# Kernel tuning notes

Measured on AMD Instinct MI355X. Metric: run time of the kernel, lower is better.

The kernel has to match this reference:

```python
import jax, jax.numpy as jnp
import numpy as np

B, S, HID = 2, 1024, 2048
N_HEADS, N_KV, HEAD_DIM = 32, 4, 128
BLOCK, MAX_BLOCKS = 32, 128
EPS = 1e-6
ROPE_THETA = 1e6


def _rmsnorm(x, w):
    # per-head RMSNorm over head_dim (Qwen3MoeRMSNorm)
    var = jnp.mean(x * x, axis=-1, keepdims=True)
    return x * jax.lax.rsqrt(var + EPS) * w


def _rotate_half(x):
    h = x.shape[-1] // 2
    return jnp.concatenate([-x[..., h:], x[..., :h]], axis=-1)


def setup_inputs() -> dict:
    key = jax.random.key(0)
    ks = jax.random.split(key, 8)
    hidden_states = jax.random.normal(ks[0], (B, S, HID), dtype=jnp.float32)
    wq = jax.random.normal(ks[1], (N_HEADS * HEAD_DIM, HID), dtype=jnp.float32) * 0.02
    wk = jax.random.normal(ks[2], (N_KV * HEAD_DIM, HID), dtype=jnp.float32) * 0.02
    wv = jax.random.normal(ks[3], (N_KV * HEAD_DIM, HID), dtype=jnp.float32) * 0.02
    wo = jax.random.normal(ks[4], (HID, N_HEADS * HEAD_DIM), dtype=jnp.float32) * 0.02
    q_norm_w = 1.0 + 0.01 * jax.random.normal(ks[5], (HEAD_DIM,), dtype=jnp.float32)
    k_norm_w = 1.0 + 0.01 * jax.random.normal(ks[6], (HEAD_DIM,), dtype=jnp.float32)
    # RoPE tables (rotate-half / llama convention)
    inv_freq = 1.0 / (ROPE_THETA ** (jnp.arange(0, HEAD_DIM, 2, dtype=jnp.float32) / HEAD_DIM))
    t = jnp.arange(S, dtype=jnp.float32)
    freqs = jnp.outer(t, inv_freq)  # [S, HEAD_DIM/2]
    emb = jnp.concatenate([freqs, freqs], axis=-1)  # [S, HEAD_DIM]
    cos, sin = jnp.cos(emb), jnp.sin(emb)
    # page table: B sequences x (S/BLOCK) blocks, distinct block ids
    page_table = jnp.arange(B * (S // BLOCK), dtype=jnp.int32).reshape(B, S // BLOCK)
    return {"hidden_states": hidden_states, "wq": wq, "wk": wk, "wv": wv, "wo": wo,
            "q_norm_w": q_norm_w, "k_norm_w": k_norm_w, "cos": cos, "sin": sin,
            "page_table": page_table}


def reference(hidden_states, wq, wk, wv, wo, q_norm_w, k_norm_w, cos, sin, page_table):
    b, s, _ = hidden_states.shape
    # fused QKV projection (math-equivalent to the concatenated qkv_proj_weight)
    q = (hidden_states @ wq.T).reshape(b, s, N_HEADS, HEAD_DIM)
    k = (hidden_states @ wk.T).reshape(b, s, N_KV, HEAD_DIM)
    v = (hidden_states @ wv.T).reshape(b, s, N_KV, HEAD_DIM)
    # per-head RMSNorm then RoPE
    q = _rmsnorm(q, q_norm_w)
    k = _rmsnorm(k, k_norm_w)
    c = cos[None, :, None, :]
    sn = sin[None, :, None, :]
    q = q * c + _rotate_half(q) * sn
    k = k * c + _rotate_half(k) * sn
    # paged KV-cache fill: [B, nblk, BLOCK, kvh, hd] -> cache[block_id, kvh, BLOCK, hd]
    nblk = s // BLOCK
    k_blk = k.reshape(b, nblk, BLOCK, N_KV, HEAD_DIM).transpose(0, 1, 3, 2, 4).reshape(-1, N_KV, BLOCK, HEAD_DIM)
    v_blk = v.reshape(b, nblk, BLOCK, N_KV, HEAD_DIM).transpose(0, 1, 3, 2, 4).reshape(-1, N_KV, BLOCK, HEAD_DIM)
    flat_pt = page_table.reshape(-1)
    cache_k = jnp.zeros((MAX_BLOCKS, N_KV, BLOCK, HEAD_DIM), dtype=k.dtype).at[flat_pt].set(k_blk)
    cache_v = jnp.zeros((MAX_BLOCKS, N_KV, BLOCK, HEAD_DIM), dtype=v.dtype).at[flat_pt].set(v_blk)
    # GQA: repeat kv heads (num_key_value_groups = 8)
    groups = N_HEADS // N_KV
    k_rep = jnp.repeat(k, groups, axis=2)  # [b, s, N_HEADS, hd]
    v_rep = jnp.repeat(v, groups, axis=2)
    # causal SDPA, scaling = head_dim ** -0.5
    scale = HEAD_DIM ** -0.5
    scores = jnp.einsum('bqhd,bkhd->bhqk', q, k_rep) * scale
    causal = jnp.tril(jnp.ones((s, s), dtype=bool))
    scores = jnp.where(causal[None, None], scores, jnp.finfo(scores.dtype).min)
    probs = jax.nn.softmax(scores, axis=-1)
    attn = jnp.einsum('bhqk,bkhd->bqhd', probs, v_rep).reshape(b, s, N_HEADS * HEAD_DIM)
    out = attn @ wo.T  # [b, s, HID]
    return out, cache_k, cache_v
```

## Files before the change

### kernel.cpp

```cpp
#include <hip/hip_runtime.h>
#include <hip/hip_bf16.h>


typedef __attribute__((ext_vector_type(8))) __bf16 bf16x8;
typedef __attribute__((ext_vector_type(4))) __bf16 bf16x4;
typedef __attribute__((ext_vector_type(4))) float f32x4;

__device__ __forceinline__ void gload16(const void* g, void* l) {
    __builtin_amdgcn_global_load_lds((const __attribute__((address_space(1))) void*)g,
                                     (__attribute__((address_space(3))) void*)l, 16, 0, 0);
}

__global__ __launch_bounds__(256) void cvt5(const float* __restrict__ s0, const float* __restrict__ s1,
                                            const float* __restrict__ s2, const float* __restrict__ s3,
                                            const float* __restrict__ s4,
                                            __bf16* __restrict__ d0, __bf16* __restrict__ d1,
                                            __bf16* __restrict__ d2, __bf16* __restrict__ d3,
                                            __bf16* __restrict__ d4) {
    const int b = blockIdx.x;
    const float* src; __bf16* dst; int off;
    if (b < 4096)       { src = s0; dst = d0; off = b; }
    else if (b < 12288) { src = s1; dst = d1; off = b - 4096; }
    else if (b < 13312) { src = s2; dst = d2; off = b - 12288; }
    else if (b < 14336) { src = s3; dst = d3; off = b - 13312; }
    else                { src = s4; dst = d4; off = b - 14336; }
    const int i = off * 256 + threadIdx.x;
    float4 v = reinterpret_cast<const float4*>(src)[i];
    bf16x4 o = {(__bf16)v.x, (__bf16)v.y, (__bf16)v.z, (__bf16)v.w};
    reinterpret_cast<bf16x4*>(dst)[i] = o;
}

__global__ __launch_bounds__(256) void reduce_add(float* __restrict__ o,
                                                  const float* __restrict__ p, int n4) {
    int i = blockIdx.x * 256 + threadIdx.x;
    int stride = gridDim.x * 256;
    for (; i < n4; i += stride) {
        float4 a = reinterpret_cast<float4*>(o)[i];
        float4 b = reinterpret_cast<const float4*>(p)[i];
        a.x += b.x; a.y += b.y; a.z += b.z; a.w += b.w;
        reinterpret_cast<float4*>(o)[i] = a;
    }
}

template <int NF, int OUT_BF16>
__global__ __launch_bounds__(512, 2) void gemm4p(const __bf16* __restrict__ A,
                                                 const __bf16* __restrict__ B,
                                                 void* __restrict__ C0,
                                                 void* __restrict__ C1,
                                                 const int M, const int N, const int K,
                                                 const int nTiles, const int nbn,
                                                 const int klen) {
    __shared__ __bf16 Asm[2 * 128 * 64];
    __shared__ __bf16 Bsm[2 * NF * 64 * 64];
    const int tid = threadIdx.x, lane = tid & 63, wave = tid >> 6;
    const int wm = wave >> 2, wn = wave & 3;
    const int lrow = lane & 15, lkg = lane >> 4;
    const int rsw = lrow & 7;
    const int bid = blockIdx.x;
    const int kz = bid / nTiles, tile = bid % nTiles;
    const int tswz = (tile & 7) * (nTiles >> 3) + (tile >> 3);
    const int bm = tswz / nbn, bn = tswz % nbn;
    const int brow = bm * 128, bcol = bn * (NF * 64);
    const int kbeg = kz * klen;
    const int row0 = tid >> 3;
    const int scol_sw = ((tid & 7) ^ (row0 & 7)) * 8;
    const __bf16* gA = A + (size_t)(brow + row0) * K + kbeg + scol_sw;
    const __bf16* gB = B + (size_t)(bcol + row0) * K + kbeg + scol_sw;
    const int slot0 = (lkg ^ rsw) * 8;
    const int slot1 = ((4 + lkg) ^ rsw) * 8;
    const int nt = klen / 64;
    constexpr int UPT = NF + 2;

    f32x4 acc[4][NF] = {};

    int su_t = 0, su_w = 0;
    auto stage1 = [&]() {
        if (su_t < nt) {
            const size_t ko = (size_t)su_t * 64;
            if (su_w < 2)
                gload16(gA + (size_t)(su_w * 64) * K + ko,
                        Asm + (su_t & 1) * 8192 + su_w * 4096 + tid * 8);
            else
                gload16(gB + (size_t)((su_w - 2) * 64) * K + ko,
                        Bsm + (su_t & 1) * (NF * 4096) + (su_w - 2) * 4096 + tid * 8);
        }
        if (++su_w == UPT) { su_w = 0; ++su_t; }
    };

    for (int u = 0; u < 2 * UPT; ++u) stage1();
    if constexpr (NF == 5) asm volatile("s_waitcnt vmcnt(7)" ::: "memory");
    else                   asm volatile("s_waitcnt vmcnt(6)" ::: "memory");
    __builtin_amdgcn_s_barrier();

    for (int t = 0; t < nt; ++t) {
        const __bf16* As = Asm + (t & 1) * 8192;
        const __bf16* Bs = Bsm + (t & 1) * (NF * 4096);
        bf16x8 ar[4], br[NF];
#pragma unroll
        for (int mi = 0; mi < 4; ++mi)
            ar[mi] = *reinterpret_cast<const bf16x8*>(&As[(wm * 64 + mi * 16 + lrow) * 64 + slot0]);
#pragma unroll
        for (int nf = 0; nf < NF; ++nf)
            br[nf] = *reinterpret_cast<const bf16x8*>(&Bs[(wn * (NF * 16) + nf * 16 + lrow) * 64 + slot0]);
        asm volatile("s_waitcnt lgkmcnt(0)" ::: "memory");
        __builtin_amdgcn_sched_barrier(0);
        __builtin_amdgcn_s_setprio(1);
#pragma unroll
        for (int mi = 0; mi < 4; ++mi)
#pragma unroll
            for (int nf = 0; nf < NF; ++nf)
                acc[mi][nf] = __builtin_amdgcn_mfma_f32_16x16x32_bf16(ar[mi], br[nf], acc[mi][nf], 0, 0, 0);
        __builtin_amdgcn_s_setprio(0);
        __builtin_amdgcn_s_barrier();
#pragma unroll
        for (int mi = 0; mi < 4; ++mi)
            ar[mi] = *reinterpret_cast<const bf16x8*>(&As[(wm * 64 + mi * 16 + lrow) * 64 + slot1]);
#pragma unroll
        for (int nf = 0; nf < NF; ++nf)
            br[nf] = *reinterpret_cast<const bf16x8*>(&Bs[(wn * (NF * 16) + nf * 16 + lrow) * 64 + slot1]);
        asm volatile("s_waitcnt lgkmcnt(0)" ::: "memory");
#pragma unroll
        for (int u = 0; u < UPT; ++u) stage1();
        __builtin_amdgcn_sched_barrier(0);
        __builtin_amdgcn_s_setprio(1);
#pragma unroll
        for (int mi = 0; mi < 4; ++mi)
#pragma unroll
            for (int nf = 0; nf < NF; ++nf)
                acc[mi][nf] = __builtin_amdgcn_mfma_f32_16x16x32_bf16(ar[mi], br[nf], acc[mi][nf], 0, 0, 0);
        __builtin_amdgcn_s_setprio(0);
        if (t + 2 < nt) {
            if constexpr (NF == 5) asm volatile("s_waitcnt vmcnt(7)" ::: "memory");
            else                   asm volatile("s_waitcnt vmcnt(6)" ::: "memory");
        } else {
            asm volatile("s_waitcnt vmcnt(0)" ::: "memory");
        }
        __builtin_amdgcn_s_barrier();
    }

    void* C = (kz == 0) ? C0 : C1;
#pragma unroll
    for (int mi = 0; mi < 4; ++mi)
#pragma unroll
        for (int nf = 0; nf < NF; ++nf)
#pragma unroll
            for (int j = 0; j < 4; ++j) {
                const size_t r = brow + wm * 64 + mi * 16 + lkg * 4 + j;
                const size_t c = bcol + wn * (NF * 16) + nf * 16 + lrow;
                if (OUT_BF16)
                    ((__bf16*)C)[r * N + c] = (__bf16)acc[mi][nf][j];
                else
                    ((float*)C)[r * N + c] = acc[mi][nf][j];
            }
}

__global__ __launch_bounds__(256) void norm_rope_cache(
    __bf16* __restrict__ qkv, const float* __restrict__ cosT, const float* __restrict__ sinT,
    const float* __restrict__ qw, const float* __restrict__ kw,
    const int* __restrict__ ptab, float* __restrict__ cacheK, float* __restrict__ cacheV) {
    const int t = blockIdx.x;
    const int b = t >> 10, s = t & 1023;
    const int wave = threadIdx.x >> 6, lane = threadIdx.x & 63;
    __bf16* row = qkv + (size_t)t * 5120;
    const float c = cosT[s * 128 + lane];
    const float sn = sinT[s * 128 + lane];
    const int page = ptab[b * 32 + (s >> 5)];
    const int so = s & 31;
    const float wq0 = qw[lane], wq1 = qw[lane + 64];
#pragma unroll
    for (int i = 0; i < 8; ++i) {
        const int h = wave * 8 + i;
        float x0 = (float)row[h * 128 + lane];
        float x1 = (float)row[h * 128 + 64 + lane];
        float ss = x0 * x0 + x1 * x1;
        for (int off = 32; off; off >>= 1) ss += __shfl_xor(ss, off);
        const float rs = rsqrtf(ss * (1.0f / 128.0f) + 1e-6f);
        const float y0 = x0 * rs * wq0, y1 = x1 * rs * wq1;
        row[h * 128 + lane]      = (__bf16)(y0 * c - y1 * sn);
        row[h * 128 + 64 + lane] = (__bf16)(y1 * c + y0 * sn);
    }
    {
        const int h = wave;
        float x0 = (float)row[4096 + h * 128 + lane];
        float x1 = (float)row[4096 + h * 128 + 64 + lane];
        float ss = x0 * x0 + x1 * x1;
        for (int off = 32; off; off >>= 1) ss += __shfl_xor(ss, off);
        const float rs = rsqrtf(ss * (1.0f / 128.0f) + 1e-6f);
        const float y0 = x0 * rs * kw[lane], y1 = x1 * rs * kw[lane + 64];
        const float o0 = y0 * c - y1 * sn, o1 = y1 * c + y0 * sn;
        row[4096 + h * 128 + lane]      = (__bf16)o0;
        row[4096 + h * 128 + 64 + lane] = (__bf16)o1;
        float* ck = cacheK + (((size_t)page * 4 + h) * 32 + so) * 128;
        ck[lane] = o0; ck[lane + 64] = o1;
        const float v0 = (float)row[4608 + h * 128 + lane];
        const float v1 = (float)row[4608 + h * 128 + 64 + lane];
        float* cv = cacheV + (((size_t)page * 4 + h) * 32 + so) * 128;
        cv[lane] = v0; cv[lane + 64] = v1;
    }
}

__global__ __launch_bounds__(256, 2) void attn_fwd(const __bf16* __restrict__ qkv,
                                                   __bf16* __restrict__ out) {
    __shared__ __bf16 Ks[2][64 * 128];
    __shared__ __bf16 Vs[2][128 * 64];
    __shared__ __bf16 Ps[4][16 * 64];
    const int qa = blockIdx.x;
    const int qbig = 63 - qa;
    const int yy = blockIdx.y;
    const int kvg = yy >> 1, hh = yy & 1;
    const int b = blockIdx.z;
    const int tid = threadIdx.x, wave = tid >> 6, lane = tid & 63;
    const int lrow = lane & 15, lkg = lane >> 4;
    const int h = kvg * 8 + hh * 4 + wave;
    const size_t base = (size_t)b * 1024 * 5120;
    const int kofs = 4096 + kvg * 128, vofs = 4608 + kvg * 128;
    const int ntA = qa / 4 + 1, nt = qbig / 4 + 1;
    const int qposA = qa * 16 + lrow, qposB = qbig * 16 + lrow;
    const int rsw = lrow & 7;

    bf16x8 aqA[4], aqB[4];
#pragma unroll
    for (int kc = 0; kc < 4; ++kc) {
        bf16x8 ta = *reinterpret_cast<const bf16x8*>(
            &qkv[base + (size_t)(qa * 16 + lrow) * 5120 + h * 128 + kc * 32 + lkg * 8]);
        bf16x8 tb = *reinterpret_cast<const bf16x8*>(
            &qkv[base + (size_t)(qbig * 16 + lrow) * 5120 + h * 128 + kc * 32 + lkg * 8]);
#pragma unroll
        for (int i = 0; i < 8; ++i) {
            ta[i] = (__bf16)((float)ta[i] * 0.08838834764831845f);
            tb[i] = (__bf16)((float)tb[i] * 0.08838834764831845f);
        }
        aqA[kc] = ta; aqB[kc] = tb;
    }

    f32x4 accA[8] = {}, accB[8] = {};
    float mA = -1e30f, lA = 0.f, mB = -1e30f, lB = 0.f;
    __bf16* Pw = &Ps[wave][0];

    auto stageK = [&](int t, int buf) {
        const int kv0 = (t < nt) ? t * 64 : 0;
#pragma unroll
        for (int c = 0; c < 4; ++c) {
            const int chunk = c * 4 + wave;
            const int row = chunk * 4 + (lane >> 4);
            const int gslot = (lane & 15) ^ (row & 7);
            gload16(&qkv[base + (size_t)(kv0 + row) * 5120 + kofs + gslot * 8],
                    &Ks[buf][chunk * 512]);
        }
    };
    auto loadV = [&](int t, uint4 (&vr)[4]) {
        const int kv0 = (t < nt) ? t * 64 : 0;
#pragma unroll
        for (int r = 0; r < 4; ++r)
            vr[r] = *reinterpret_cast<const uint4*>(
                &qkv[base + (size_t)(kv0 + lane) * 5120 + vofs + wave * 32 + r * 8]);
    };
    auto writeV = [&](uint4 (&vr)[4], int buf) {
#pragma unroll
        for (int r = 0; r < 4; ++r) {
            const __bf16* pv = reinterpret_cast<const __bf16*>(&vr[r]);
#pragma unroll
            for (int j = 0; j < 8; ++j) {
                const int d = wave * 32 + r * 8 + j;
                Vs[buf][d * 64 + (((lane >> 3) ^ j) << 3) + (lane & 7)] = pv[j];
            }
        }
    };

    auto smax = [&](f32x4 (&st)[4], float& m_i, float& l_i, f32x4 (&acc)[8],
                    int qpos, int kv0, bool maskit) {
        float sv[16]; float pmax = -1e30f;
#pragma unroll
        for (int f = 0; f < 4; ++f)
#pragma unroll
            for (int j = 0; j < 4; ++j) {
                float x = st[f][j];
                if (maskit) {
                    const int kvpos = kv0 + f * 16 + lkg * 4 + j;
                    if (kvpos > qpos) x = -1e30f;
                }
                sv[f * 4 + j] = x;
                pmax = fmaxf(pmax, x);
            }
        pmax = fmaxf(pmax, __shfl_xor(pmax, 16));
        pmax = fmaxf(pmax, __shfl_xor(pmax, 32));
        if (!__all(pmax - m_i <= 8.f)) {
            const float m_new = fmaxf(m_i, pmax);
            const float sf = __expf(m_i - m_new);
            m_i = m_new;
            l_i *= sf;
            float sfj[4];
#pragma unroll
            for (int j = 0; j < 4; ++j) sfj[j] = __shfl(sf, lkg * 4 + j);
#pragma unroll
            for (int f = 0; f < 8; ++f)
#pragma unroll
                for (int j = 0; j < 4; ++j) acc[f][j] *= sfj[j];
        }
        float ladd = 0.f;
#pragma unroll
        for (int f = 0; f < 4; ++f) {
            bf16x4 pb;
#pragma unroll
            for (int j = 0; j < 4; ++j) {
                const float p = __expf(sv[f * 4 + j] - m_i);
                ladd += p;
                pb[j] = (__bf16)p;
            }
            const int slot = (f * 2 + (lkg >> 1)) ^ rsw;
            *reinterpret_cast<bf16x4*>(&Pw[lrow * 64 + slot * 8 + (lkg & 1) * 4]) = pb;
        }
        ladd += __shfl_xor(ladd, 16);
        ladd += __shfl_xor(ladd, 32);
        l_i += ladd;
    };

    auto pv = [&](f32x4 (&acc)[8], int kbuf) {
#pragma unroll
        for (int kk = 0; kk < 2; ++kk) {
            const int pslot = ((kk * 4 + lkg) ^ rsw) << 3;
            bf16x8 ap = *reinterpret_cast<const bf16x8*>(&Pw[lrow * 64 + pslot]);
#pragma unroll
            for (int f = 0; f < 8; ++f) {
                bf16x8 bv = *reinterpret_cast<const bf16x8*>(
                    &Vs[kbuf][(f * 16 + lrow) * 64 + pslot]);
                acc[f] = __builtin_amdgcn_mfma_f32_16x16x32_bf16(ap, bv, acc[f], 0, 0, 0);
            }
        }
    };

    auto body = [&](int t, uint4 (&vcur)[4], uint4 (&vnext)[4]) {
        const int kbuf = t & 1;
        __builtin_amdgcn_s_barrier();
        asm volatile("" ::: "memory");
        loadV(t + 1, vnext);
        stageK(t + 1, kbuf ^ 1);
        asm volatile("s_waitcnt vmcnt(8)" ::: "memory");
        writeV(vcur, kbuf);
        asm volatile("s_waitcnt lgkmcnt(0)" ::: "memory");
        __builtin_amdgcn_s_barrier();
        asm volatile("" ::: "memory");

        const bool doA = t < ntA;
        f32x4 stA[4] = {}, stB[4] = {};
#pragma unroll
        for (int kc = 0; kc < 4; ++kc)
#pragma unroll
            for (int f = 0; f < 4; ++f) {
                bf16x8 ak = *reinterpret_cast<const bf16x8*>(
                    &Ks[kbuf][(f * 16 + lrow) * 128 + (((kc * 4 + lkg) ^ rsw) << 3)]);
                stB[f] = __builtin_amdgcn_mfma_f32_16x16x32_bf16(ak, aqB[kc], stB[f], 0, 0, 0);
                if (doA)
                    stA[f] = __builtin_amdgcn_mfma_f32_16x16x32_bf16(ak, aqA[kc], stA[f], 0, 0, 0);
            }
        if (doA) {
            smax(stA, mA, lA, accA, qposA, t * 64, t == ntA - 1);
            pv(accA, kbuf);
        }
        smax(stB, mB, lB, accB, qposB, t * 64, t == nt - 1);
        pv(accB, kbuf);
    };

    uint4 vrA[4], vrB[4];
    loadV(0, vrA);
    stageK(0, 0);
    for (int t = 0; t < nt; t += 2) {
        body(t, vrA, vrB);
        if (t + 1 < nt) body(t + 1, vrB, vrA);
    }
    asm volatile("s_waitcnt vmcnt(0)" ::: "memory");

    float linvA[4], linvB[4];
#pragma unroll
    for (int j = 0; j < 4; ++j) {
        linvA[j] = 1.0f / __shfl(lA, lkg * 4 + j);
        linvB[j] = 1.0f / __shfl(lB, lkg * 4 + j);
    }
#pragma unroll
    for (int f = 0; f < 8; ++f)
#pragma unroll
        for (int j = 0; j < 4; ++j) {
            out[((size_t)b * 1024 + qa * 16 + lkg * 4 + j) * 4096 + h * 128 + f * 16 + lrow] =
                (__bf16)(accA[f][j] * linvA[j]);
            out[((size_t)b * 1024 + qbig * 16 + lkg * 4 + j) * 4096 + h * 128 + f * 16 + lrow] =
                (__bf16)(accB[f][j] * linvB[j]);
        }
}

extern "C" void kernel_launch(void* const* d_in, const int* in_sizes, int n_in,
                              void* d_out, int out_size, void* d_ws, size_t ws_size,
                              hipStream_t stream) {
    const float* hidden = (const float*)d_in[0];
    const float* wq = (const float*)d_in[1];
    const float* wk = (const float*)d_in[2];
    const float* wv = (const float*)d_in[3];
    const float* wo = (const float*)d_in[4];
    const float* qnw = (const float*)d_in[5];
    const float* knw = (const float*)d_in[6];
    const float* cosT = (const float*)d_in[7];
    const float* sinT = (const float*)d_in[8];
    const int* ptab = (const int*)d_in[9];

    float* outp = (float*)d_out;
    float* cacheK = outp + 4194304;
    float* cacheV = cacheK + 2097152;

    char* ws = (char*)d_ws;
    __bf16* hbf    = (__bf16*)ws;
    __bf16* w1bf   = (__bf16*)(ws + 8388608);
    __bf16* wobf   = (__bf16*)(ws + 29360128);
    __bf16* qkvbf  = (__bf16*)(ws + 46137344);
    __bf16* attnbf = (__bf16*)ws;
    float*  opart  = (float*)(ws + 46137344);

    cvt5<<<22528, 256, 0, stream>>>(hidden, wq, wk, wv, wo,
                                    hbf, w1bf, w1bf + (size_t)4096 * 2048,
                                    w1bf + (size_t)4608 * 2048, wobf);

    gemm4p<5, 1><<<256, 512, 0, stream>>>(hbf, w1bf, qkvbf, nullptr,
                                          2048, 5120, 2048, 256, 16, 2048);

    hipMemsetAsync(cacheK, 0, (size_t)4194304 * 4, stream);
    norm_rope_cache<<<2048, 256, 0, stream>>>(qkvbf, cosT, sinT, qnw, knw, ptab, cacheK, cacheV);

    attn_fwd<<<dim3(32, 8, 2), 256, 0, stream>>>(qkvbf, attnbf);

    gemm4p<4, 0><<<256, 512, 0, stream>>>(attnbf, wobf, outp, opart,
                                          2048, 2048, 4096, 128, 8, 2048);
    reduce_add<<<2048, 256, 0, stream>>>(outp, opart, 4194304 / 4);
}
```

Measured before the change: 213.0 us.

## Share K/V tiles across all eight GQA heads per block with 512 threads

The attention kernel now launches 512-thread blocks with eight waves, so one block covers all eight query heads of a KV group instead of four. Each K/V tile is staged into shared memory once for eight heads rather than twice, which halves redundant global K/V traffic and staging work per wave. The PV stage is also merged so the A and B query tiles share each V fragment load, using separate P buffers. The cost is half as many blocks in the grid (256 instead of 512) and more registers and LDS per block, which may lower occupancy and parallelism on a large GPU.

```diff
diff --git a/kernel.cpp b/kernel.cpp
--- a/kernel.cpp
+++ b/kernel.cpp
@@ -199,19 +199,17 @@
     }
 }
 
-__global__ __launch_bounds__(256, 2) void attn_fwd(const __bf16* __restrict__ qkv,
+__global__ __launch_bounds__(512, 2) void attn_fwd(const __bf16* __restrict__ qkv,
                                                    __bf16* __restrict__ out) {
     __shared__ __bf16 Ks[2][64 * 128];
     __shared__ __bf16 Vs[2][128 * 64];
-    __shared__ __bf16 Ps[4][16 * 64];
+    __shared__ __bf16 Ps[8][2][16 * 64];
     const int qa = blockIdx.x;
     const int qbig = 63 - qa;
-    const int yy = blockIdx.y;
-    const int kvg = yy >> 1, hh = yy & 1;
-    const int b = blockIdx.z;
+    const int kvg = blockIdx.y, b = blockIdx.z;
     const int tid = threadIdx.x, wave = tid >> 6, lane = tid & 63;
     const int lrow = lane & 15, lkg = lane >> 4;
-    const int h = kvg * 8 + hh * 4 + wave;
+    const int h = kvg * 8 + wave;
     const size_t base = (size_t)b * 1024 * 5120;
     const int kofs = 4096 + kvg * 128, vofs = 4608 + kvg * 128;
     const int ntA = qa / 4 + 1, nt = qbig / 4 + 1;
@@ -235,40 +233,41 @@
 
     f32x4 accA[8] = {}, accB[8] = {};
     float mA = -1e30f, lA = 0.f, mB = -1e30f, lB = 0.f;
-    __bf16* Pw = &Ps[wave][0];
+    __bf16* PwA = &Ps[wave][0][0];
+    __bf16* PwB = &Ps[wave][1][0];
 
     auto stageK = [&](int t, int buf) {
         const int kv0 = (t < nt) ? t * 64 : 0;
 #pragma unroll
-        for (int c = 0; c < 4; ++c) {
-            const int chunk = c * 4 + wave;
+        for (int c = 0; c < 2; ++c) {
+            const int chunk = c * 8 + wave;
             const int row = chunk * 4 + (lane >> 4);
             const int gslot = (lane & 15) ^ (row & 7);
             gload16(&qkv[base + (size_t)(kv0 + row) * 5120 + kofs + gslot * 8],
                     &Ks[buf][chunk * 512]);
         }
     };
-    auto loadV = [&](int t, uint4 (&vr)[4]) {
+    auto loadV = [&](int t, uint4 (&vr)[2]) {
         const int kv0 = (t < nt) ? t * 64 : 0;
 #pragma unroll
-        for (int r = 0; r < 4; ++r)
+        for (int r = 0; r < 2; ++r)
             vr[r] = *reinterpret_cast<const uint4*>(
-                &qkv[base + (size_t)(kv0 + lane) * 5120 + vofs + wave * 32 + r * 8]);
-    };
-    auto writeV = [&](uint4 (&vr)[4], int buf) {
-#pragma unroll
-        for (int r = 0; r < 4; ++r) {
+                &qkv[base + (size_t)(kv0 + lane) * 5120 + vofs + wave * 16 + r * 8]);
+    };
+    auto writeV = [&](uint4 (&vr)[2], int buf) {
+#pragma unroll
+        for (int r = 0; r < 2; ++r) {
             const __bf16* pv = reinterpret_cast<const __bf16*>(&vr[r]);
 #pragma unroll
             for (int j = 0; j < 8; ++j) {
-                const int d = wave * 32 + r * 8 + j;
+                const int d = wave * 16 + r * 8 + j;
                 Vs[buf][d * 64 + (((lane >> 3) ^ j) << 3) + (lane & 7)] = pv[j];
             }
         }
     };
 
     auto smax = [&](f32x4 (&st)[4], float& m_i, float& l_i, f32x4 (&acc)[8],
-                    int qpos, int kv0, bool maskit) {
+                    int qpos, int kv0, bool maskit, __bf16* Pw) {
         float sv[16]; float pmax = -1e30f;
 #pragma unroll
         for (int f = 0; f < 4; ++f)
@@ -315,27 +314,13 @@
         l_i += ladd;
     };
 
-    auto pv = [&](f32x4 (&acc)[8], int kbuf) {
-#pragma unroll
-        for (int kk = 0; kk < 2; ++kk) {
-            const int pslot = ((kk * 4 + lkg) ^ rsw) << 3;
-            bf16x8 ap = *reinterpret_cast<const bf16x8*>(&Pw[lrow * 64 + pslot]);
-#pragma unroll
-            for (int f = 0; f < 8; ++f) {
-                bf16x8 bv = *reinterpret_cast<const bf16x8*>(
-                    &Vs[kbuf][(f * 16 + lrow) * 64 + pslot]);
-                acc[f] = __builtin_amdgcn_mfma_f32_16x16x32_bf16(ap, bv, acc[f], 0, 0, 0);
-            }
-        }
-    };
-
-    auto body = [&](int t, uint4 (&vcur)[4], uint4 (&vnext)[4]) {
+    auto body = [&](int t, uint4 (&vcur)[2], uint4 (&vnext)[2]) {
         const int kbuf = t & 1;
         __builtin_amdgcn_s_barrier();
         asm volatile("" ::: "memory");
         loadV(t + 1, vnext);
         stageK(t + 1, kbuf ^ 1);
-        asm volatile("s_waitcnt vmcnt(8)" ::: "memory");
+        asm volatile("s_waitcnt vmcnt(4)" ::: "memory");
         writeV(vcur, kbuf);
         asm volatile("s_waitcnt lgkmcnt(0)" ::: "memory");
         __builtin_amdgcn_s_barrier();
@@ -353,15 +338,26 @@
                 if (doA)
                     stA[f] = __builtin_amdgcn_mfma_f32_16x16x32_bf16(ak, aqA[kc], stA[f], 0, 0, 0);
             }
-        if (doA) {
-            smax(stA, mA, lA, accA, qposA, t * 64, t == ntA - 1);
-            pv(accA, kbuf);
-        }
-        smax(stB, mB, lB, accB, qposB, t * 64, t == nt - 1);
-        pv(accB, kbuf);
-    };
-
-    uint4 vrA[4], vrB[4];
+        if (doA) smax(stA, mA, lA, accA, qposA, t * 64, t == ntA - 1, PwA);
+        smax(stB, mB, lB, accB, qposB, t * 64, t == nt - 1, PwB);
+#pragma unroll
+        for (int kk = 0; kk < 2; ++kk) {
+            const int pslot = ((kk * 4 + lkg) ^ rsw) << 3;
+            bf16x8 apB = *reinterpret_cast<const bf16x8*>(&PwB[lrow * 64 + pslot]);
+            bf16x8 apA;
+            if (doA) apA = *reinterpret_cast<const bf16x8*>(&PwA[lrow * 64 + pslot]);
+#pragma unroll
+            for (int f = 0; f < 8; ++f) {
+                bf16x8 bv = *reinterpret_cast<const bf16x8*>(
+                    &Vs[kbuf][(f * 16 + lrow) * 64 + pslot]);
+                accB[f] = __builtin_amdgcn_mfma_f32_16x16x32_bf16(apB, bv, accB[f], 0, 0, 0);
+                if (doA)
+                    accA[f] = __builtin_amdgcn_mfma_f32_16x16x32_bf16(apA, bv, accA[f], 0, 0, 0);
+            }
+        }
+    };
+
+    uint4 vrA[2], vrB[2];
     loadV(0, vrA);
     stageK(0, 0);
     for (int t = 0; t < nt; t += 2) {
@@ -423,7 +419,7 @@
     hipMemsetAsync(cacheK, 0, (size_t)4194304 * 4, stream);
     norm_rope_cache<<<2048, 256, 0, stream>>>(qkvbf, cosT, sinT, qnw, knw, ptab, cacheK, cacheV);
 
-    attn_fwd<<<dim3(32, 8, 2), 256, 0, stream>>>(qkvbf, attnbf);
+    attn_fwd<<<dim3(32, 4, 2), 512, 0, stream>>>(qkvbf, attnbf);
 
     gemm4p<4, 0><<<256, 512, 0, stream>>>(attnbf, wobf, outp, opart,
                                           2048, 2048, 4096, 128, 8, 2048);
```

After: 193.3 us. 9.3% less time.

## Share each KV tile across all eight GQA heads with 512-thread attention blocks

Applied to the files above, without the earlier changes.

The attention kernel now runs eight waves per block, one per query head in a GQA group, so each K/V tile is loaded once for all eight heads instead of twice across two four-wave blocks. KV tiles grow from 64 to 128 rows and are processed in two 64-row halves, with per-half causal skipping. V is now single-buffered, with separate P buffers for the A and B query tiles. The grid flattens to 256 blocks with group-major block ordering. This halves redundant global K/V traffic, at the cost of larger LDS use, fewer blocks and possible occupancy limits.

```diff
diff --git a/kernel.cpp b/kernel.cpp
--- a/kernel.cpp
+++ b/kernel.cpp
@@ -199,22 +199,23 @@
     }
 }
 
-__global__ __launch_bounds__(256, 2) void attn_fwd(const __bf16* __restrict__ qkv,
+__global__ __launch_bounds__(512, 2) void attn_fwd(const __bf16* __restrict__ qkv,
                                                    __bf16* __restrict__ out) {
-    __shared__ __bf16 Ks[2][64 * 128];
-    __shared__ __bf16 Vs[2][128 * 64];
-    __shared__ __bf16 Ps[4][16 * 64];
-    const int qa = blockIdx.x;
+    __shared__ __bf16 Ks[2][128 * 128];
+    __shared__ __bf16 Vs[128 * 128];
+    __shared__ __bf16 Ps[8][2][16 * 64];
+    const int bid = blockIdx.x;
+    const int qa = bid >> 3;
+    const int g = bid & 7;
+    const int kvg = g & 3, b = g >> 2;
     const int qbig = 63 - qa;
-    const int yy = blockIdx.y;
-    const int kvg = yy >> 1, hh = yy & 1;
-    const int b = blockIdx.z;
     const int tid = threadIdx.x, wave = tid >> 6, lane = tid & 63;
     const int lrow = lane & 15, lkg = lane >> 4;
-    const int h = kvg * 8 + hh * 4 + wave;
+    const int h = kvg * 8 + wave;
     const size_t base = (size_t)b * 1024 * 5120;
     const int kofs = 4096 + kvg * 128, vofs = 4608 + kvg * 128;
-    const int ntA = qa / 4 + 1, nt = qbig / 4 + 1;
+    const int ntA = qa / 8 + 1, nt = qbig / 8 + 1;
+    const int lastA = qa >> 2, lastB = qbig >> 2;
     const int qposA = qa * 16 + lrow, qposB = qbig * 16 + lrow;
     const int rsw = lrow & 7;
 
@@ -235,13 +236,14 @@
 
     f32x4 accA[8] = {}, accB[8] = {};
     float mA = -1e30f, lA = 0.f, mB = -1e30f, lB = 0.f;
-    __bf16* Pw = &Ps[wave][0];
+    __bf16* PwA = &Ps[wave][0][0];
+    __bf16* PwB = &Ps[wave][1][0];
 
     auto stageK = [&](int t, int buf) {
-        const int kv0 = (t < nt) ? t * 64 : 0;
+        const int kv0 = (t < nt) ? t * 128 : 0;
 #pragma unroll
         for (int c = 0; c < 4; ++c) {
-            const int chunk = c * 4 + wave;
+            const int chunk = c * 8 + wave;
             const int row = chunk * 4 + (lane >> 4);
             const int gslot = (lane & 15) ^ (row & 7);
             gload16(&qkv[base + (size_t)(kv0 + row) * 5120 + kofs + gslot * 8],
@@ -249,26 +251,31 @@
         }
     };
     auto loadV = [&](int t, uint4 (&vr)[4]) {
-        const int kv0 = (t < nt) ? t * 64 : 0;
-#pragma unroll
-        for (int r = 0; r < 4; ++r)
+        const int kv0 = (t < nt) ? t * 128 : 0;
+#pragma unroll
+        for (int r = 0; r < 4; ++r) {
+            const int kv = (r & 1) * 64 + lane;
+            const int d0 = wave * 16 + (r >> 1) * 8;
             vr[r] = *reinterpret_cast<const uint4*>(
-                &qkv[base + (size_t)(kv0 + lane) * 5120 + vofs + wave * 32 + r * 8]);
-    };
-    auto writeV = [&](uint4 (&vr)[4], int buf) {
+                &qkv[base + (size_t)(kv0 + kv) * 5120 + vofs + d0]);
+        }
+    };
+    auto writeV = [&](uint4 (&vr)[4]) {
 #pragma unroll
         for (int r = 0; r < 4; ++r) {
             const __bf16* pv = reinterpret_cast<const __bf16*>(&vr[r]);
+            const int kv = (r & 1) * 64 + lane;
+            const int slot = kv >> 3, klo = kv & 7;
 #pragma unroll
             for (int j = 0; j < 8; ++j) {
-                const int d = wave * 32 + r * 8 + j;
-                Vs[buf][d * 64 + (((lane >> 3) ^ j) << 3) + (lane & 7)] = pv[j];
+                const int d = wave * 16 + (r >> 1) * 8 + j;
+                Vs[d * 128 + ((slot ^ (d & 7)) << 3) + klo] = pv[j];
             }
         }
     };
 
     auto smax = [&](f32x4 (&st)[4], float& m_i, float& l_i, f32x4 (&acc)[8],
-                    int qpos, int kv0, bool maskit) {
+                    int qpos, int kv0, bool maskit, __bf16* Pw) {
         float sv[16]; float pmax = -1e30f;
 #pragma unroll
         for (int f = 0; f < 4; ++f)
@@ -315,7 +322,7 @@
         l_i += ladd;
     };
 
-    auto pv = [&](f32x4 (&acc)[8], int kbuf) {
+    auto pvH = [&](f32x4 (&acc)[8], int hf, __bf16* Pw) {
 #pragma unroll
         for (int kk = 0; kk < 2; ++kk) {
             const int pslot = ((kk * 4 + lkg) ^ rsw) << 3;
@@ -323,7 +330,7 @@
 #pragma unroll
             for (int f = 0; f < 8; ++f) {
                 bf16x8 bv = *reinterpret_cast<const bf16x8*>(
-                    &Vs[kbuf][(f * 16 + lrow) * 64 + pslot]);
+                    &Vs[(f * 16 + lrow) * 128 + hf * 64 + pslot]);
                 acc[f] = __builtin_amdgcn_mfma_f32_16x16x32_bf16(ap, bv, acc[f], 0, 0, 0);
             }
         }
@@ -336,29 +343,40 @@
         loadV(t + 1, vnext);
         stageK(t + 1, kbuf ^ 1);
         asm volatile("s_waitcnt vmcnt(8)" ::: "memory");
-        writeV(vcur, kbuf);
+        writeV(vcur);
         asm volatile("s_waitcnt lgkmcnt(0)" ::: "memory");
         __builtin_amdgcn_s_barrier();
         asm volatile("" ::: "memory");
 
         const bool doA = t < ntA;
-        f32x4 stA[4] = {}, stB[4] = {};
-#pragma unroll
-        for (int kc = 0; kc < 4; ++kc)
-#pragma unroll
-            for (int f = 0; f < 4; ++f) {
-                bf16x8 ak = *reinterpret_cast<const bf16x8*>(
-                    &Ks[kbuf][(f * 16 + lrow) * 128 + (((kc * 4 + lkg) ^ rsw) << 3)]);
-                stB[f] = __builtin_amdgcn_mfma_f32_16x16x32_bf16(ak, aqB[kc], stB[f], 0, 0, 0);
-                if (doA)
-                    stA[f] = __builtin_amdgcn_mfma_f32_16x16x32_bf16(ak, aqA[kc], stA[f], 0, 0, 0);
-            }
-        if (doA) {
-            smax(stA, mA, lA, accA, qposA, t * 64, t == ntA - 1);
-            pv(accA, kbuf);
-        }
-        smax(stB, mB, lB, accB, qposB, t * 64, t == nt - 1);
-        pv(accB, kbuf);
+#pragma unroll
+        for (int hf = 0; hf < 2; ++hf) {
+            const int kh = 2 * t + hf;
+            const bool actA = doA && (kh <= lastA);
+            const bool actB = kh <= lastB;
+            if (!actB && !actA) continue;
+            f32x4 stA[4] = {}, stB[4] = {};
+#pragma unroll
+            for (int kc = 0; kc < 4; ++kc)
+#pragma unroll
+                for (int f = 0; f < 4; ++f) {
+                    bf16x8 ak = *reinterpret_cast<const bf16x8*>(
+                        &Ks[kbuf][(hf * 64 + f * 16 + lrow) * 128 + (((kc * 4 + lkg) ^ rsw) << 3)]);
+                    if (actB)
+                        stB[f] = __builtin_amdgcn_mfma_f32_16x16x32_bf16(ak, aqB[kc], stB[f], 0, 0, 0);
+                    if (actA)
+                        stA[f] = __builtin_amdgcn_mfma_f32_16x16x32_bf16(ak, aqA[kc], stA[f], 0, 0, 0);
+                }
+            const int kv0 = t * 128 + hf * 64;
+            if (actA) {
+                smax(stA, mA, lA, accA, qposA, kv0, kh == lastA, PwA);
+                pvH(accA, hf, PwA);
+            }
+            if (actB) {
+                smax(stB, mB, lB, accB, qposB, kv0, kh == lastB, PwB);
+                pvH(accB, hf, PwB);
+            }
+        }
     };
 
     uint4 vrA[4], vrB[4];
@@ -423,7 +441,7 @@
     hipMemsetAsync(cacheK, 0, (size_t)4194304 * 4, stream);
     norm_rope_cache<<<2048, 256, 0, stream>>>(qkvbf, cosT, sinT, qnw, knw, ptab, cacheK, cacheV);
 
-    attn_fwd<<<dim3(32, 8, 2), 256, 0, stream>>>(qkvbf, attnbf);
+    attn_fwd<<<256, 512, 0, stream>>>(qkvbf, attnbf);
 
     gemm4p<4, 0><<<256, 512, 0, stream>>>(attnbf, wobf, outp, opart,
                                           2048, 2048, 4096, 128, 8, 2048);
```

Measured after the change: 192.1 us. -9.8%, faster.
